# Performance work log

Measured on AMD Instinct MI355X. Metric: run time of the kernel, lower is better.

The kernel has to match this reference:

```python
import jax, jax.numpy as jnp
import numpy as np

PYRAMID_LEVEL = 3

def _ceil_div(a, b):
    return -(-a // b)

def build_region_masks(H, W, levels=PYRAMID_LEVEL):
    """Binary region-membership matrices per pyramid level (overlap=True).
    Level l has (2**l)**2 overlapping windows; sum-pooling over a window equals
    a matmul with these masks (zero padding contributes nothing)."""
    Ms = []
    for level in range(levels):
        ns = 2 ** level
        h_wid = _ceil_div(2 * H, ns + 1); w_wid = _ceil_div(2 * W, ns + 1)
        h_str = _ceil_div(H, ns + 1);     w_str = _ceil_div(W, ns + 1)
        H_new = h_wid + (ns - 1) * h_str; W_new = w_wid + (ns - 1) * w_str
        pad_top = (H_new - H) // 2; pad_left = (W_new - W) // 2
        M = np.zeros((ns * ns, H, W), np.float32)
        r = 0
        for i in range(ns):
            for j in range(ns):
                h0 = i * h_str - pad_top; w0 = j * w_str - pad_left
                M[r, max(h0, 0):min(h0 + h_wid, H), max(w0, 0):min(w0 + w_wid, W)] = 1.0
                r += 1
        Ms.append(M.reshape(ns * ns, H * W))
    return Ms

def setup_inputs() -> dict:
    key = jax.random.key(0)
    ks = jax.random.split(key, 6)
    N, C, H, W, K, S, L = 32, 128, 48, 48, 64, 4, 3
    return {
        "x": jax.random.normal(ks[0], (N, C, H, W), jnp.float32),
        "centroids": jax.random.uniform(ks[1], (K, C), dtype=jnp.float32),
        "conv_w": jax.random.normal(ks[2], (K, C), jnp.float32) * 0.1,
        "conv_shadow_w": jax.random.normal(ks[3], (K * S, C), jnp.float32) * 0.1,
        "conv_app_w": jax.random.normal(ks[4], (L, K, C), jnp.float32) * 0.1,
        "cluster_weights": jnp.ones((K,), jnp.float32),
    }

def reference(x, centroids, conv_w, conv_shadow_w, conv_app_w, cluster_weights):
    N, C, H, W = x.shape
    K = centroids.shape[0]
    S = conv_shadow_w.shape[0] // K
    L = conv_app_w.shape[0]
    P = H * W
    eps = 1e-12
    # descriptor-wise L2 normalization of input
    x = x / jnp.maximum(jnp.linalg.norm(x, axis=1, keepdims=True), eps)
    xp = x.reshape(N, C, P)
    # 1x1-conv soft assignment (no bias, vladv2=False)
    score = jnp.einsum('kc,ncp->nkp', conv_w, xp)            # [N,K,P]
    a = jax.nn.softmax(score, axis=1)                        # over clusters
    # shadow weighting: each cluster competes with its S shadow clusters
    sh = jnp.einsum('kc,ncp->nkp', conv_shadow_w, xp).reshape(N, K, S, P)
    cat = jnp.concatenate([score[:, :, None, :], sh], axis=2)  # [N,K,1+S,P]
    sal_pix = jax.nn.softmax(cat, axis=2)[:, :, 0, :]          # salient prob
    a = a * sal_pix                                            # [N,K,P]
    # attentional pyramid saliency: per-level 1x1 conv + relu + region sum-pool
    Ms = build_region_masks(H, W, L)
    sal = jnp.concatenate([
        jnp.einsum('nkp,rp->nkr',
                   jax.nn.relu(jnp.einsum('kc,ncp->nkp', conv_app_w[l], xp)),
                   jnp.asarray(Ms[l]))
        for l in range(L)], axis=2)                            # [N,K,R], R=21
    Mall = jnp.asarray(np.concatenate(Ms, axis=0))             # [R,P]
    # fused pyramid aggregation: sum_r sal_r * sumpool_r((x - c_k) * a_k)
    # == contraction with per-pixel weight w = M^T @ sal
    w = jnp.einsum('nkr,rp->nkp', sal, Mall)                   # [N,K,P]
    aw = a * w
    vlad = jnp.einsum('nkp,ncp->nkc', aw, xp) - centroids[None] * aw.sum(-1)[..., None]
    # intra (per-cluster) L2 normalization
    vlad = vlad / jnp.maximum(jnp.linalg.norm(vlad, axis=2, keepdims=True), eps)
    # parametric normalization
    vlad = vlad * cluster_weights[None, :, None]
    v = vlad.reshape(N, K * C)
    return v / jnp.maximum(jnp.linalg.norm(v, axis=1, keepdims=True), eps)
```

## Files before the change

### kernel.cpp

```cpp
#include <hip/hip_runtime.h>
#include <hip/hip_bf16.h>

#define N_ 32
#define C_ 128
#define H_ 48
#define W_ 48
#define P_ (H_*W_)
#define K_ 64
#define S_ 4
#define L_ 3
#define R_ 21
#define NB_ 72
#define M_ 512
#define CH_ 9
#define CHV_ 18

typedef __hip_bfloat16 bf16;
typedef __attribute__((ext_vector_type(8))) short   bf16x8;
typedef __attribute__((ext_vector_type(8))) unsigned short u16x8;
typedef __attribute__((ext_vector_type(4))) float   f32x4;

__device__ __forceinline__ float b2f(bf16 v){ return __bfloat162float(v); }
__device__ __forceinline__ float u2f(unsigned short u){
  union { unsigned i; float f; } v; v.i = ((unsigned)u) << 16; return v.f;
}
__device__ __forceinline__ unsigned short f2u(float f){
  bf16 h = __float2bfloat16(f);
  return *(unsigned short*)&h;
}

__device__ __forceinline__ int is_f32(const unsigned short* __restrict__ xb){
  int lane = threadIdx.x & 63;
  int w = 0;
  #pragma unroll
  for (int i=0;i<16;++i){
    int e = (xb[lane*16 + i] >> 7) & 0xFF;
    w += (e >= 0x8E) ? 1 : 0;
  }
  unsigned long long b = __ballot(w > 0);
  return __popcll(b) > 32;
}

__device__ __forceinline__ unsigned short region_bit(int r, int h, int w){
  bool m;
  if (r == 0){
    m = true;
  } else if (r < 5){
    int q = r-1, i = q>>1, j = q&1;
    m = (h>=16*i)&&(h<16*i+32)&&(w>=16*j)&&(w<16*j+32);
  } else if (r < 21){
    int q = r-5, i = q>>2, j = q&3;
    m = (h>=10*i-1)&&(h<10*i+19)&&(w>=10*j-1)&&(w<10*j+19);
  } else {
    m = false;
  }
  return m ? (unsigned short)0x3F80 : (unsigned short)0;
}

__global__ __launch_bounds__(256) void k_wall(const void* __restrict__ cvw, const void* __restrict__ csw,
                                              const void* __restrict__ caw, const void* __restrict__ x,
                                              bf16* __restrict__ WallF){
  int f32 = is_f32((const unsigned short*)x);
  int i = blockIdx.x*256 + threadIdx.x;
  int j = i&7, lane = (i>>3)&63, ks = (i>>9)&3, rt = (i>>11)&7, wv = (i>>14)&3;
  int row = wv*128 + rt*16 + (lane&15);
  int c   = ks*32 + ((lane>>4)&3)*8 + j;
  int s = row*C_ + c;
  float v;
  if (s < 8192)       v = f32 ? ((const float*)cvw)[s]        : b2f(((const bf16*)cvw)[s]);
  else if (s < 40960) v = f32 ? ((const float*)csw)[s-8192]   : b2f(((const bf16*)csw)[s-8192]);
  else                v = f32 ? ((const float*)caw)[s-40960]  : b2f(((const bf16*)caw)[s-40960]);
  WallF[i] = __float2bfloat16(v);
}

__global__ __launch_bounds__(256) void k_norm(const void* __restrict__ x,
                                              bf16* __restrict__ xnF,
                                              bf16* __restrict__ xnG){
  __shared__ float sred[2][128];
  __shared__ __align__(16) unsigned short tile[128][136];
  int f32 = is_f32((const unsigned short*)x);
  int bi = blockIdx.x;
  int n = bi / (P_/128), tb = bi % (P_/128);
  int p0 = tb*128;
  int t = threadIdx.x, px = t&127, chh = t>>7, c0 = chh*64;

  float vals[64];
  float ss = 0.f;
  if (f32){
    const float* xb = (const float*)x + ((size_t)n*C_ + c0)*P_ + p0 + px;
    #pragma unroll
    for (int j=0;j<64;++j){ float v = xb[(size_t)j*P_]; vals[j] = v; ss += v*v; }
  } else {
    const unsigned short* xb = (const unsigned short*)x + ((size_t)n*C_ + c0)*P_ + p0 + px;
    #pragma unroll
    for (int j=0;j<64;++j){ float v = u2f(xb[(size_t)j*P_]); vals[j] = v; ss += v*v; }
  }
  sred[chh][px] = ss;
  __syncthreads();
  float invn = 1.f / fmaxf(sqrtf(sred[0][px] + sred[1][px]), 1e-12f);
  unsigned short nv[64];
  #pragma unroll
  for (int j=0;j<64;++j) nv[j] = f2u(vals[j]*invn);

  #pragma unroll
  for (int j=0;j<64;++j) tile[c0+j][px] = nv[j];
  __syncthreads();
  {
    int ch = tb>>1, hb = tb&1;
    size_t gbase = ((size_t)(n*CH_ + ch)*8 + hb*4)*512;
    u16x8* out = (u16x8*)xnG;
    #pragma unroll
    for (int it=0;it<8;++it){
      int o2 = t + it*256;
      int lane = o2&63, half = (o2>>6)&1, wvv = (o2>>7)&3, ksl = (o2>>9)&3;
      int c  = wvv*32 + half*16 + (lane&15);
      int pl = ksl*32 + ((lane>>4)&3)*8;
      out[gbase + o2] = *(const u16x8*)&tile[c][pl];
    }
  }
  __syncthreads();
  #pragma unroll
  for (int j8=0;j8<8;++j8)
    *(u16x8*)&tile[px][c0 + j8*8] = *(const u16x8*)&nv[j8*8];
  __syncthreads();
  {
    size_t fbase = (size_t)(n*NB_ + tb*4)*512;
    u16x8* out = (u16x8*)xnF;
    #pragma unroll
    for (int it=0;it<8;++it){
      int o = t + it*256;
      int lane = o&63, half = (o>>6)&1, ks = (o>>7)&3, pbl = (o>>9)&3;
      int pxr = pbl*32 + half*16 + (lane&15);
      int cc  = ks*32 + ((lane>>4)&3)*8;
      out[fbase + o] = *(const u16x8*)&tile[pxr][cc];
    }
  }
}

__global__ __launch_bounds__(256, 4) void k_gemm(const bf16* __restrict__ WallF,
                                                 const bf16* __restrict__ xnF,
                                                 unsigned short* __restrict__ a,
                                                 float* __restrict__ salPart){
  __shared__ __align__(16) unsigned short ldsU[320][40];
  unsigned short (*appS)[40] = ldsU;
  int n = blockIdx.y, pb = blockIdx.x;
  int p0 = pb*32;
  int t = threadIdx.x, wv = t>>6, l = t&63;
  int mrow = l&15, quad = l>>4;

  const bf16* Af = WallF + ((size_t)(wv*8)*4)*512 + l*8;
  const bf16* Bf = xnF + (size_t)(n*NB_ + pb)*4096 + l*8;

  f32x4 acc[8][2];
  #pragma unroll
  for (int rt=0;rt<8;++rt){ acc[rt][0] = (f32x4){0,0,0,0}; acc[rt][1] = (f32x4){0,0,0,0}; }

  #pragma unroll
  for (int ks=0;ks<4;++ks){
    bf16x8 b0 = *(const bf16x8*)(Bf + (ks*2+0)*512);
    bf16x8 b1 = *(const bf16x8*)(Bf + (ks*2+1)*512);
    #pragma unroll
    for (int rt=0;rt<8;++rt){
      bf16x8 af = *(const bf16x8*)(Af + (rt*4+ks)*512);
      acc[rt][0] = __builtin_amdgcn_mfma_f32_16x16x32_bf16(af, b0, acc[rt][0], 0,0,0);
      acc[rt][1] = __builtin_amdgcn_mfma_f32_16x16x32_bf16(af, b1, acc[rt][1], 0,0,0);
    }
  }

  unsigned appPk[8][2][2];
  #pragma unroll
  for (int rt=0;rt<8;++rt){
    int row0 = wv*128 + rt*16;
    if (row0 < 64){
      #pragma unroll
      for (int ct=0;ct<2;++ct)
        #pragma unroll
        for (int r=0;r<4;++r)
          ldsU[row0 + quad*4 + r][ct*16 + mrow] = f2u(acc[rt][ct][r]);
    } else if (row0 < 320){
      #pragma unroll
      for (int ct=0;ct<2;++ct)
        #pragma unroll
        for (int r=0;r<4;++r){
          int sr = row0 + quad*4 + r - 64;
          ldsU[64 + (sr&3)*64 + (sr>>2)][ct*16 + mrow] = f2u(acc[rt][ct][r]);
        }
    } else {
      #pragma unroll
      for (int ct=0;ct<2;++ct){
        appPk[rt][ct][0] = (unsigned)f2u(fmaxf(acc[rt][ct][0],0.f))
                         | ((unsigned)f2u(fmaxf(acc[rt][ct][1],0.f)) << 16);
        appPk[rt][ct][1] = (unsigned)f2u(fmaxf(acc[rt][ct][2],0.f))
                         | ((unsigned)f2u(fmaxf(acc[rt][ct][3],0.f)) << 16);
      }
    }
  }
  __syncthreads();

  {
    int pg = wv;
    u16x8 s8  = *(const u16x8*)&ldsU[l      ][pg*8];
    u16x8 h0v = *(const u16x8*)&ldsU[64  + l][pg*8];
    u16x8 h1v = *(const u16x8*)&ldsU[128 + l][pg*8];
    u16x8 h2v = *(const u16x8*)&ldsU[192 + l][pg*8];
    u16x8 h3v = *(const u16x8*)&ldsU[256 + l][pg*8];
    float ez[8], Zr[8];
    #pragma unroll
    for (int j=0;j<8;++j){ ez[j] = __expf(u2f((unsigned short)s8[j])); Zr[j] = ez[j]; }
    #pragma unroll
    for (int st=1; st<64; st<<=1){
      #pragma unroll
      for (int j=0;j<8;++j) Zr[j] += __shfl_xor(Zr[j], st);
    }
    size_t tile = (size_t)n*NB_ + pb;
    #pragma unroll
    for (int j=0;j<8;++j){
      float e0 = ez[j];
      float den = e0 + __expf(u2f((unsigned short)h0v[j]))
                     + __expf(u2f((unsigned short)h1v[j]))
                     + __expf(u2f((unsigned short)h2v[j]))
                     + __expf(u2f((unsigned short)h3v[j]));
      a[tile*2048 + (size_t)(pg*8+j)*64 + l] = f2u(__fdividef(e0*e0, Zr[j]*den));
    }
  }
  __syncthreads();

  #pragma unroll
  for (int rt=0;rt<8;++rt){
    int row0 = wv*128 + rt*16;
    if (row0 >= 320){
      int ar0 = row0 - 320 + quad*4;
      #pragma unroll
      for (int ct=0;ct<2;++ct){
        appS[ar0+0][ct*16+mrow] = (unsigned short)(appPk[rt][ct][0] & 0xffff);
        appS[ar0+1][ct*16+mrow] = (unsigned short)(appPk[rt][ct][0] >> 16);
        appS[ar0+2][ct*16+mrow] = (unsigned short)(appPk[rt][ct][1] & 0xffff);
        appS[ar0+3][ct*16+mrow] = (unsigned short)(appPk[rt][ct][1] >> 16);
      }
    }
  }
  __syncthreads();

  bf16x8 bm0, bm1;
  #pragma unroll
  for (int j=0;j<8;++j){
    int p = p0 + quad*8 + j;
    int h = p/48, wc = p - h*48;
    bm0[j] = (short)region_bit(mrow,      h, wc);
    bm1[j] = (short)region_bit(16 + mrow, h, wc);
  }
  f32x4 racc[3][2];
  #pragma unroll
  for (int i=0;i<3;++i){ racc[i][0] = (f32x4){0,0,0,0}; racc[i][1] = (f32x4){0,0,0,0}; }
  #pragma unroll
  for (int i=0;i<3;++i){
    int rt = wv*3 + i;
    bf16x8 af = *(const bf16x8*)&appS[rt*16 + mrow][quad*8];
    racc[i][0] = __builtin_amdgcn_mfma_f32_16x16x32_bf16(af, bm0, racc[i][0], 0,0,0);
    racc[i][1] = __builtin_amdgcn_mfma_f32_16x16x32_bf16(af, bm1, racc[i][1], 0,0,0);
  }
  {
    size_t tile = (size_t)n*NB_ + pb;
    float* sp = salPart + tile*(K_*R_);
    #pragma unroll
    for (int i=0;i<3;++i){
      int rt = wv*3 + i;
      int kb = rt*16 + quad*4;
      if (rt < 4){
        if (mrow == 0){
          #pragma unroll
          for (int r=0;r<4;++r) sp[(size_t)(kb+r)*R_] = racc[i][0][r];
        }
      } else if (rt < 8){
        if (mrow >= 1 && mrow <= 4){
          #pragma unroll
          for (int r=0;r<4;++r) sp[(size_t)(kb+r-64)*R_ + mrow] = racc[i][0][r];
        }
      } else {
        if (mrow >= 5){
          #pragma unroll
          for (int r=0;r<4;++r) sp[(size_t)(kb+r-128)*R_ + mrow] = racc[i][0][r];
        } else {
          #pragma unroll
          for (int r=0;r<4;++r) sp[(size_t)(kb+r-128)*R_ + 16 + mrow] = racc[i][1][r];
        }
      }
    }
  }
}

__global__ __launch_bounds__(256) void k_salred(const float* __restrict__ salPart,
                                                float* __restrict__ sal){
  int tid = blockIdx.x*256 + threadIdx.x;
  if (tid >= N_*K_*R_) return;
  int n = tid / (K_*R_), i = tid - n*(K_*R_);
  const float* sp = salPart + (size_t)n*NB_*(K_*R_) + i;
  float s = 0.f;
  #pragma unroll 8
  for (int b=0;b<NB_;++b) s += sp[(size_t)b*(K_*R_)];
  sal[tid] = s;
}

__global__ __launch_bounds__(512) void k_vlad(const bf16* __restrict__ xnG,
                                              const unsigned short* __restrict__ a,
                                              const float* __restrict__ sal,
                                              float* __restrict__ vladPart,
                                              float* __restrict__ sumawPart){
  __shared__ float s_sal[K_][R_];
  __shared__ __align__(16) unsigned short awL[4][K_][40];
  __shared__ float s_part[4][K_];
  int c2 = blockIdx.x, n = blockIdx.y, t = threadIdx.x;
  int p0 = c2*128;
  for (int i=t;i<K_*R_;i+=512) ((float*)s_sal)[i] = sal[(size_t)n*K_*R_ + i];
  __syncthreads();

  {
    int pxl = t & 127, kq = t>>7;
    int pbl = pxl>>5, px = pxl&31;
    int p = p0 + pxl;
    int h = p/48, wc = p - h*48;
    bool h1[2], w1[2], h2[4], w2[4];
    #pragma unroll
    for (int i=0;i<2;++i){ h1[i] = (h>=16*i)&&(h<16*i+32); w1[i] = (wc>=16*i)&&(wc<16*i+32); }
    #pragma unroll
    for (int i=0;i<4;++i){ h2[i] = (h>=10*i-1)&&(h<10*i+19); w2[i] = (wc>=10*i-1)&&(wc<10*i+19); }
    const unsigned short* at = a + ((size_t)((n*NB_ + c2*4 + pbl)*32 + px))*K_ + kq*16;
    u16x8 av[2];
    av[0] = *(const u16x8*)at;
    av[1] = *(const u16x8*)(at + 8);
    #pragma unroll
    for (int kk=0;kk<16;++kk){
      int k = kq*16 + kk;
      float w = s_sal[k][0];
      #pragma unroll
      for (int i=0;i<2;++i) if (h1[i])
        #pragma unroll
        for (int j=0;j<2;++j) if (w1[j]) w += s_sal[k][1+2*i+j];
      #pragma unroll
      for (int i=0;i<4;++i) if (h2[i])
        #pragma unroll
        for (int j=0;j<4;++j) if (w2[j]) w += s_sal[k][5+4*i+j];
      awL[pbl][k][px] = f2u(u2f(av[kk>>3][kk&7]) * w);
    }
  }
  __syncthreads();
  if (t < 256){
    int k = t&63, qr = t>>6;
    float s = 0.f;
    #pragma unroll 8
    for (int j=0;j<32;++j) s += u2f(awL[qr][k][j]);
    s_part[qr][k] = s;
  }
  __syncthreads();

  int wave = t>>6, l = t&63, mrow = l&15, quad = l>>4;
  int wvc = wave&3, mh = wave>>2;
  f32x4 acc[2][2];
  #pragma unroll
  for (int mtl=0;mtl<2;++mtl){ acc[mtl][0] = (f32x4){0,0,0,0}; acc[mtl][1] = (f32x4){0,0,0,0}; }
  const bf16* Gf = xnG + (size_t)(n*CH_ + (c2>>1))*32768 + l*8;
  int ksbase = (c2&1)*4;
  #pragma unroll
  for (int ksl=0;ksl<4;++ksl){
    int ks = ksbase + ksl;
    bf16x8 b0 = *(const bf16x8*)(Gf + ((ks*4+wvc)*2+0)*512);
    bf16x8 b1 = *(const bf16x8*)(Gf + ((ks*4+wvc)*2+1)*512);
    #pragma unroll
    for (int mtl=0;mtl<2;++mtl){
      bf16x8 af = *(const bf16x8*)((const bf16*)&awL[ksl][(mh*2+mtl)*16 + mrow][quad*8]);
      acc[mtl][0] = __builtin_amdgcn_mfma_f32_16x16x32_bf16(af, b0, acc[mtl][0], 0,0,0);
      acc[mtl][1] = __builtin_amdgcn_mfma_f32_16x16x32_bf16(af, b1, acc[mtl][1], 0,0,0);
    }
  }
  float* vp = vladPart + ((size_t)(n*CHV_ + c2))*(K_*C_);
  #pragma unroll
  for (int mtl=0;mtl<2;++mtl){
    #pragma unroll
    for (int ct=0;ct<2;++ct){
      int c = wvc*32 + ct*16 + mrow;
      #pragma unroll
      for (int r=0;r<4;++r){
        int k = (mh*2+mtl)*16 + quad*4 + r;
        vp[k*C_ + c] = acc[mtl][ct][r];
      }
    }
  }
  if (t < K_){
    float s = s_part[0][t] + s_part[1][t] + s_part[2][t] + s_part[3][t];
    sumawPart[((size_t)n*CHV_ + c2)*K_ + t] = s;
  }
}

__global__ __launch_bounds__(256) void k_vred(const float* __restrict__ vladPart,
                                              const float* __restrict__ sumawPart,
                                              const void* __restrict__ cen,
                                              const void* __restrict__ x,
                                              float* __restrict__ vlad){
  int f32 = is_f32((const unsigned short*)x);
  int tid = blockIdx.x*256 + threadIdx.x;
  int n = tid >> 13;
  int i = tid & 8191;
  int k = i >> 7;
  const float* vp = vladPart + (size_t)n*CHV_*(K_*C_) + i;
  float s = 0.f;
  #pragma unroll
  for (int ch=0;ch<CHV_;++ch) s += vp[(size_t)ch*(K_*C_)];
  float sw = 0.f;
  #pragma unroll
  for (int ch=0;ch<CHV_;++ch) sw += sumawPart[((size_t)n*CHV_ + ch)*K_ + k];
  float cv = f32 ? ((const float*)cen)[i] : b2f(((const bf16*)cen)[i]);
  vlad[tid] = s - cv*sw;
}

__global__ __launch_bounds__(256) void k_final(const float* __restrict__ vlad,
                                               const void* __restrict__ clw,
                                               const void* __restrict__ x,
                                               void* __restrict__ out){
  __shared__ float s_v[K_*C_];
  __shared__ float s_ssk[K_];
  __shared__ float s_scale[K_];
  __shared__ float s_gs;
  int n = blockIdx.x, t = threadIdx.x;
  int f32 = is_f32((const unsigned short*)x);
  const float* vp = vlad + (size_t)n*K_*C_;
  for (int i=t;i<K_*C_;i+=256) s_v[i] = vp[i];
  __syncthreads();
  int k = t >> 2, q = t & 3;
  float ss = 0.f;
  for (int mm=0;mm<32;++mm){ float v = s_v[k*C_ + q + 4*mm]; ss += v*v; }
  ss += __shfl_down(ss, 2);
  ss += __shfl_down(ss, 1);
  if (q == 0) s_ssk[k] = ss;
  __syncthreads();
  if (t < K_){
    float cw = f32 ? ((const float*)clw)[t] : b2f(((const bf16*)clw)[t]);
    s_scale[t] = cw / fmaxf(sqrtf(s_ssk[t]), 1e-12f);
  }
  __syncthreads();
  if (t == 0){
    float gss = 0.f;
    for (int kk=0;kk<K_;++kk) gss += s_ssk[kk]*s_scale[kk]*s_scale[kk];
    s_gs = 1.f / fmaxf(sqrtf(gss), 1e-12f);
  }
  __syncthreads();
  float gsc = s_gs;
  if (f32){
    float* op = (float*)out + (size_t)n*K_*C_;
    for (int i=t;i<K_*C_;i+=256) op[i] = s_v[i]*s_scale[i>>7]*gsc;
  } else {
    bf16* op = (bf16*)out + (size_t)n*K_*C_;
    for (int i=t;i<K_*C_;i+=256) op[i] = __float2bfloat16(s_v[i]*s_scale[i>>7]*gsc);
  }
}

extern "C" void kernel_launch(void* const* d_in, const int* in_sizes, int n_in,
                              void* d_out, int out_size, void* d_ws, size_t ws_size,
                              hipStream_t stream){
  const void* x   = d_in[0];
  const void* cen = d_in[1];
  const void* cvw = d_in[2];
  const void* csw = d_in[3];
  const void* caw = d_in[4];
  const void* clw = d_in[5];

  char* ws = (char*)d_ws;
  bf16* WallF = (bf16*)ws;             ws += (size_t)M_*C_*2;
  bf16* xnF   = (bf16*)ws;             ws += (size_t)N_*P_*C_*2;
  bf16* xnG   = (bf16*)ws;             ws += (size_t)N_*C_*P_*2;
  char* aBuf  = ws;                    ws += (size_t)N_*K_*P_*2;
  unsigned short* a = (unsigned short*)aBuf;
  float* vlad = (float*)aBuf;
  float* sal  = (float*)ws;            ws += (size_t)N_*K_*R_*4;
  char* un = ws;
  float* salPart   = (float*)un;
  float* sumawPart = (float*)un;
  ws += (size_t)N_*NB_*K_*R_*4;
  float* vladPart = (float*)xnF;

  k_wall  <<<dim3(M_*C_/256),       256, 0, stream>>>(cvw, csw, caw, x, WallF);
  k_norm  <<<dim3(N_*P_/128),       256, 0, stream>>>(x, xnF, xnG);
  k_gemm  <<<dim3(NB_, N_),         256, 0, stream>>>(WallF, xnF, a, salPart);
  k_salred<<<dim3((N_*K_*R_+255)/256), 256, 0, stream>>>(salPart, sal);
  k_vlad  <<<dim3(CHV_, N_),        512, 0, stream>>>(xnG, a, sal, vladPart, sumawPart);
  k_vred  <<<dim3(N_*K_*C_/256),    256, 0, stream>>>(vladPart, sumawPart, cen, x, vlad);
  k_final <<<dim3(N_),              256, 0, stream>>>(vlad, clw, x, d_out);
}
```

Measured before the change: 164.0 us.

## Split k_gemm across eight waves and give app activations separate LDS buffer

k_gemm now runs with 512 threads (8 waves), each computing 64 output rows instead of 128, and the WallF layout is re-indexed to match. The relu'd app-conv results go straight into a separate LDS array rather than being packed into registers and written back after a barrier, which removes one __syncthreads. The softmax stage handles 4 pixels per wave, and the region-pool MFMA work is spread unevenly across waves. The aim is lower register pressure and more latency hiding per block, at the cost of more LDS per block and some idle waves in the pooling phase.

New measurement: 153.5 us. -6.4%, faster.

```diff
diff --git a/kernel.cpp b/kernel.cpp
--- a/kernel.cpp
+++ b/kernel.cpp
@@ -18,6 +18,7 @@
 typedef __hip_bfloat16 bf16;
 typedef __attribute__((ext_vector_type(8))) short   bf16x8;
 typedef __attribute__((ext_vector_type(8))) unsigned short u16x8;
+typedef __attribute__((ext_vector_type(4))) unsigned short u16x4;
 typedef __attribute__((ext_vector_type(4))) float   f32x4;
 
 __device__ __forceinline__ float b2f(bf16 v){ return __bfloat162float(v); }
@@ -62,8 +63,8 @@
                                               bf16* __restrict__ WallF){
   int f32 = is_f32((const unsigned short*)x);
   int i = blockIdx.x*256 + threadIdx.x;
-  int j = i&7, lane = (i>>3)&63, ks = (i>>9)&3, rt = (i>>11)&7, wv = (i>>14)&3;
-  int row = wv*128 + rt*16 + (lane&15);
+  int j = i&7, lane = (i>>3)&63, ks = (i>>9)&3, rt = (i>>11)&31;
+  int row = rt*16 + (lane&15);
   int c   = ks*32 + ((lane>>4)&3)*8 + j;
   int s = row*C_ + c;
   float v;
@@ -137,154 +138,139 @@
   }
 }
 
-__global__ __launch_bounds__(256, 4) void k_gemm(const bf16* __restrict__ WallF,
+__global__ __launch_bounds__(512, 4) void k_gemm(const bf16* __restrict__ WallF,
                                                  const bf16* __restrict__ xnF,
                                                  unsigned short* __restrict__ a,
                                                  float* __restrict__ salPart){
   __shared__ __align__(16) unsigned short ldsU[320][40];
-  unsigned short (*appS)[40] = ldsU;
+  __shared__ __align__(16) unsigned short appS[192][40];
   int n = blockIdx.y, pb = blockIdx.x;
   int p0 = pb*32;
-  int t = threadIdx.x, wv = t>>6, l = t&63;
+  int t = threadIdx.x, w = t>>6, l = t&63;
   int mrow = l&15, quad = l>>4;
 
-  const bf16* Af = WallF + ((size_t)(wv*8)*4)*512 + l*8;
+  const bf16* Af = WallF + ((size_t)(w*4)*4)*512 + l*8;
   const bf16* Bf = xnF + (size_t)(n*NB_ + pb)*4096 + l*8;
 
-  f32x4 acc[8][2];
-  #pragma unroll
-  for (int rt=0;rt<8;++rt){ acc[rt][0] = (f32x4){0,0,0,0}; acc[rt][1] = (f32x4){0,0,0,0}; }
+  f32x4 acc[4][2];
+  #pragma unroll
+  for (int rtl=0;rtl<4;++rtl){ acc[rtl][0] = (f32x4){0,0,0,0}; acc[rtl][1] = (f32x4){0,0,0,0}; }
 
   #pragma unroll
   for (int ks=0;ks<4;++ks){
     bf16x8 b0 = *(const bf16x8*)(Bf + (ks*2+0)*512);
     bf16x8 b1 = *(const bf16x8*)(Bf + (ks*2+1)*512);
     #pragma unroll
-    for (int rt=0;rt<8;++rt){
-      bf16x8 af = *(const bf16x8*)(Af + (rt*4+ks)*512);
-      acc[rt][0] = __builtin_amdgcn_mfma_f32_16x16x32_bf16(af, b0, acc[rt][0], 0,0,0);
-      acc[rt][1] = __builtin_amdgcn_mfma_f32_16x16x32_bf16(af, b1, acc[rt][1], 0,0,0);
-    }
-  }
-
-  unsigned appPk[8][2][2];
-  #pragma unroll
-  for (int rt=0;rt<8;++rt){
-    int row0 = wv*128 + rt*16;
+    for (int rtl=0;rtl<4;++rtl){
+      bf16x8 af = *(const bf16x8*)(Af + (rtl*4+ks)*512);
+      acc[rtl][0] = __builtin_amdgcn_mfma_f32_16x16x32_bf16(af, b0, acc[rtl][0], 0,0,0);
+      acc[rtl][1] = __builtin_amdgcn_mfma_f32_16x16x32_bf16(af, b1, acc[rtl][1], 0,0,0);
+    }
+  }
+
+  #pragma unroll
+  for (int rtl=0;rtl<4;++rtl){
+    int row0 = w*64 + rtl*16;
     if (row0 < 64){
       #pragma unroll
       for (int ct=0;ct<2;++ct)
         #pragma unroll
         for (int r=0;r<4;++r)
-          ldsU[row0 + quad*4 + r][ct*16 + mrow] = f2u(acc[rt][ct][r]);
+          ldsU[row0 + quad*4 + r][ct*16 + mrow] = f2u(acc[rtl][ct][r]);
     } else if (row0 < 320){
       #pragma unroll
       for (int ct=0;ct<2;++ct)
         #pragma unroll
         for (int r=0;r<4;++r){
           int sr = row0 + quad*4 + r - 64;
-          ldsU[64 + (sr&3)*64 + (sr>>2)][ct*16 + mrow] = f2u(acc[rt][ct][r]);
+          ldsU[64 + (sr&3)*64 + (sr>>2)][ct*16 + mrow] = f2u(acc[rtl][ct][r]);
         }
     } else {
-      #pragma unroll
-      for (int ct=0;ct<2;++ct){
-        appPk[rt][ct][0] = (unsigned)f2u(fmaxf(acc[rt][ct][0],0.f))
-                         | ((unsigned)f2u(fmaxf(acc[rt][ct][1],0.f)) << 16);
-        appPk[rt][ct][1] = (unsigned)f2u(fmaxf(acc[rt][ct][2],0.f))
-                         | ((unsigned)f2u(fmaxf(acc[rt][ct][3],0.f)) << 16);
-      }
+      int ar0 = row0 - 320 + quad*4;
+      #pragma unroll
+      for (int ct=0;ct<2;++ct)
+        #pragma unroll
+        for (int r=0;r<4;++r)
+          appS[ar0 + r][ct*16 + mrow] = f2u(fmaxf(acc[rtl][ct][r], 0.f));
     }
   }
   __syncthreads();
 
   {
-    int pg = wv;
-    u16x8 s8  = *(const u16x8*)&ldsU[l      ][pg*8];
-    u16x8 h0v = *(const u16x8*)&ldsU[64  + l][pg*8];
-    u16x8 h1v = *(const u16x8*)&ldsU[128 + l][pg*8];
-    u16x8 h2v = *(const u16x8*)&ldsU[192 + l][pg*8];
-    u16x8 h3v = *(const u16x8*)&ldsU[256 + l][pg*8];
-    float ez[8], Zr[8];
-    #pragma unroll
-    for (int j=0;j<8;++j){ ez[j] = __expf(u2f((unsigned short)s8[j])); Zr[j] = ez[j]; }
+    u16x4 s4  = *(const u16x4*)&ldsU[l      ][w*4];
+    u16x4 h0v = *(const u16x4*)&ldsU[64  + l][w*4];
+    u16x4 h1v = *(const u16x4*)&ldsU[128 + l][w*4];
+    u16x4 h2v = *(const u16x4*)&ldsU[192 + l][w*4];
+    u16x4 h3v = *(const u16x4*)&ldsU[256 + l][w*4];
+    float ez[4], Zr[4];
+    #pragma unroll
+    for (int j=0;j<4;++j){ ez[j] = __expf(u2f((unsigned short)s4[j])); Zr[j] = ez[j]; }
     #pragma unroll
     for (int st=1; st<64; st<<=1){
       #pragma unroll
-      for (int j=0;j<8;++j) Zr[j] += __shfl_xor(Zr[j], st);
+      for (int j=0;j<4;++j) Zr[j] += __shfl_xor(Zr[j], st);
     }
     size_t tile = (size_t)n*NB_ + pb;
     #pragma unroll
-    for (int j=0;j<8;++j){
+    for (int j=0;j<4;++j){
       float e0 = ez[j];
       float den = e0 + __expf(u2f((unsigned short)h0v[j]))
                      + __expf(u2f((unsigned short)h1v[j]))
                      + __expf(u2f((unsigned short)h2v[j]))
                      + __expf(u2f((unsigned short)h3v[j]));
-      a[tile*2048 + (size_t)(pg*8+j)*64 + l] = f2u(__fdividef(e0*e0, Zr[j]*den));
-    }
-  }
-  __syncthreads();
-
-  #pragma unroll
-  for (int rt=0;rt<8;++rt){
-    int row0 = wv*128 + rt*16;
-    if (row0 >= 320){
-      int ar0 = row0 - 320 + quad*4;
-      #pragma unroll
-      for (int ct=0;ct<2;++ct){
-        appS[ar0+0][ct*16+mrow] = (unsigned short)(appPk[rt][ct][0] & 0xffff);
-        appS[ar0+1][ct*16+mrow] = (unsigned short)(appPk[rt][ct][0] >> 16);
-        appS[ar0+2][ct*16+mrow] = (unsigned short)(appPk[rt][ct][1] & 0xffff);
-        appS[ar0+3][ct*16+mrow] = (unsigned short)(appPk[rt][ct][1] >> 16);
-      }
-    }
-  }
-  __syncthreads();
-
-  bf16x8 bm0, bm1;
+      a[tile*2048 + (size_t)(w*4+j)*64 + l] = f2u(__fdividef(e0*e0, Zr[j]*den));
+    }
+  }
+
+  bf16x8 bm0;
   #pragma unroll
   for (int j=0;j<8;++j){
     int p = p0 + quad*8 + j;
     int h = p/48, wc = p - h*48;
-    bm0[j] = (short)region_bit(mrow,      h, wc);
-    bm1[j] = (short)region_bit(16 + mrow, h, wc);
-  }
-  f32x4 racc[3][2];
-  #pragma unroll
-  for (int i=0;i<3;++i){ racc[i][0] = (f32x4){0,0,0,0}; racc[i][1] = (f32x4){0,0,0,0}; }
-  #pragma unroll
-  for (int i=0;i<3;++i){
-    int rt = wv*3 + i;
-    bf16x8 af = *(const bf16x8*)&appS[rt*16 + mrow][quad*8];
-    racc[i][0] = __builtin_amdgcn_mfma_f32_16x16x32_bf16(af, bm0, racc[i][0], 0,0,0);
-    racc[i][1] = __builtin_amdgcn_mfma_f32_16x16x32_bf16(af, bm1, racc[i][1], 0,0,0);
-  }
-  {
-    size_t tile = (size_t)n*NB_ + pb;
-    float* sp = salPart + tile*(K_*R_);
-    #pragma unroll
-    for (int i=0;i<3;++i){
-      int rt = wv*3 + i;
+    bm0[j] = (short)region_bit(mrow, h, wc);
+  }
+  size_t tile = (size_t)n*NB_ + pb;
+  float* sp = salPart + tile*(K_*R_);
+  if (w < 4){
+    #pragma unroll
+    for (int i=0;i<2;++i){
+      int rt = w*2 + i;
+      bf16x8 af = *(const bf16x8*)&appS[rt*16 + mrow][quad*8];
+      f32x4 r0 = (f32x4){0,0,0,0};
+      r0 = __builtin_amdgcn_mfma_f32_16x16x32_bf16(af, bm0, r0, 0,0,0);
       int kb = rt*16 + quad*4;
       if (rt < 4){
         if (mrow == 0){
           #pragma unroll
-          for (int r=0;r<4;++r) sp[(size_t)(kb+r)*R_] = racc[i][0][r];
+          for (int r=0;r<4;++r) sp[(size_t)(kb+r)*R_] = r0[r];
         }
-      } else if (rt < 8){
+      } else {
         if (mrow >= 1 && mrow <= 4){
           #pragma unroll
-          for (int r=0;r<4;++r) sp[(size_t)(kb+r-64)*R_ + mrow] = racc[i][0][r];
-        }
-      } else {
-        if (mrow >= 5){
-          #pragma unroll
-          for (int r=0;r<4;++r) sp[(size_t)(kb+r-128)*R_ + mrow] = racc[i][0][r];
-        } else {
-          #pragma unroll
-          for (int r=0;r<4;++r) sp[(size_t)(kb+r-128)*R_ + 16 + mrow] = racc[i][1][r];
+          for (int r=0;r<4;++r) sp[(size_t)(kb+r-64)*R_ + mrow] = r0[r];
         }
       }
+    }
+  } else {
+    int rt = 8 + (w-4);
+    bf16x8 bm1;
+    #pragma unroll
+    for (int j=0;j<8;++j){
+      int p = p0 + quad*8 + j;
+      int h = p/48, wc = p - h*48;
+      bm1[j] = (short)region_bit(16 + mrow, h, wc);
+    }
+    bf16x8 af = *(const bf16x8*)&appS[rt*16 + mrow][quad*8];
+    f32x4 r0 = (f32x4){0,0,0,0}, r1 = (f32x4){0,0,0,0};
+    r0 = __builtin_amdgcn_mfma_f32_16x16x32_bf16(af, bm0, r0, 0,0,0);
+    r1 = __builtin_amdgcn_mfma_f32_16x16x32_bf16(af, bm1, r1, 0,0,0);
+    int kb = rt*16 + quad*4;
+    if (mrow >= 5){
+      #pragma unroll
+      for (int r=0;r<4;++r) sp[(size_t)(kb+r-128)*R_ + mrow] = r0[r];
+    } else {
+      #pragma unroll
+      for (int r=0;r<4;++r) sp[(size_t)(kb+r-128)*R_ + 16 + mrow] = r1[r];
     }
   }
 }
@@ -479,7 +465,7 @@
 
   k_wall  <<<dim3(M_*C_/256),       256, 0, stream>>>(cvw, csw, caw, x, WallF);
   k_norm  <<<dim3(N_*P_/128),       256, 0, stream>>>(x, xnF, xnG);
-  k_gemm  <<<dim3(NB_, N_),         256, 0, stream>>>(WallF, xnF, a, salPart);
+  k_gemm  <<<dim3(NB_, N_),         512, 0, stream>>>(WallF, xnF, a, salPart);
   k_salred<<<dim3((N_*K_*R_+255)/256), 256, 0, stream>>>(salPart, sal);
   k_vlad  <<<dim3(CHV_, N_),        512, 0, stream>>>(xnG, a, sal, vladPart, sumawPart);
   k_vred  <<<dim3(N_*K_*C_/256),    256, 0, stream>>>(vladPart, sumawPart, cen, x, vlad);
```
